# Optimization experiments

Measured on AMD Instinct MI355X. Metric: run time of the kernel, lower is better.

## Reference

```python
import jax, jax.numpy as jnp
import numpy as np

B, H, S, D = 4, 16, 2048, 64


def setup_inputs() -> dict:
    key = jax.random.key(0)
    kq, kk, kv = jax.random.split(key, 3)
    q = jax.random.normal(kq, (B, H, S, D), dtype=jnp.float32)
    k = jax.random.normal(kk, (B, H, S, D), dtype=jnp.float32)
    v = jax.random.normal(kv, (B, H, S, D), dtype=jnp.float32)
    return {"q": q, "k": k, "v": v}


def reference(q, k, v):
    d_k = q.shape[-1]
    scale = 1.0 / jnp.sqrt(jnp.asarray(d_k, dtype=q.dtype))
    # scores: [B, H, S_q, S_k]
    scores = jnp.einsum("bhqd,bhkd->bhqk", q, k) * scale
    attn = jax.nn.softmax(scores, axis=-1)
    out = jnp.einsum("bhqk,bhkd->bhqd", attn, v)
    return out
```

## Files before the change

### kernel.cpp

```cpp
#include <hip/hip_runtime.h>


#define NT 32
#define M0 10.0f

typedef unsigned short u16;
typedef unsigned int   u32;
typedef __bf16 bf16x8 __attribute__((ext_vector_type(8)));
typedef u16    u16x8  __attribute__((ext_vector_type(8)));
typedef u32    u32x4  __attribute__((ext_vector_type(4)));
typedef float  f32x16 __attribute__((ext_vector_type(16)));

__device__ __forceinline__ u16 f2bf(float f) {
    union { float f; u32 u; } x; x.f = f;
    u32 r = x.u + 0x7FFFu + ((x.u >> 16) & 1u);
    return (u16)(r >> 16);
}
__device__ __forceinline__ u32 cvt_pk_bf16(float lo, float hi) {
    u32 r; asm("v_cvt_pk_bf16_f32 %0, %1, %2" : "=v"(r) : "v"(lo), "v"(hi));
    return r;
}
__device__ __forceinline__ float fexp2(float x) {
    float r; asm("v_exp_f32 %0, %1" : "=v"(r) : "v"(x));
    return r;
}
__device__ __forceinline__ void gload16(const void* g, void* l) {
    __builtin_amdgcn_global_load_lds(
        (const __attribute__((address_space(1))) u32*)g,
        (__attribute__((address_space(3))) u32*)l, 16, 0, 0);
}

__global__ __launch_bounds__(256)
void prepass_kernel(const float* __restrict__ K, const float* __restrict__ V,
                    u16* __restrict__ Kb, u16* __restrict__ Vt)
{
    __shared__ u16 T[64 * 66];
    const int t   = threadIdx.x;
    const int bh  = blockIdx.x >> 5;
    const int s0  = (blockIdx.x & 31) * 64;
    const int row = t >> 2;
    const int c0  = (t & 3) * 16;

    {
        const float* kp = K + ((size_t)bh * 2048 + s0 + row) * 64 + c0;
        #pragma unroll
        for (int i = 0; i < 2; ++i) {
            float4 a = ((const float4*)kp)[2 * i];
            float4 b = ((const float4*)kp)[2 * i + 1];
            u16x8 o;
            o[0] = f2bf(a.x); o[1] = f2bf(a.y); o[2] = f2bf(a.z); o[3] = f2bf(a.w);
            o[4] = f2bf(b.x); o[5] = f2bf(b.y); o[6] = f2bf(b.z); o[7] = f2bf(b.w);
            *(u16x8*)(Kb + ((size_t)bh * 2048 + s0 + row) * 64 + c0 + 8 * i) = o;
        }
    }
    {
        const float* vp = V + ((size_t)bh * 2048 + s0 + row) * 64 + c0;
        #pragma unroll
        for (int i = 0; i < 4; ++i) {
            float4 a = ((const float4*)vp)[i];
            T[(c0 + 4 * i + 0) * 66 + row] = f2bf(a.x);
            T[(c0 + 4 * i + 1) * 66 + row] = f2bf(a.y);
            T[(c0 + 4 * i + 2) * 66 + row] = f2bf(a.z);
            T[(c0 + 4 * i + 3) * 66 + row] = f2bf(a.w);
        }
    }
    __syncthreads();
    {
        const int d  = t >> 2;
        const int k0 = (t & 3) * 16;
        #pragma unroll
        for (int i = 0; i < 2; ++i) {
            u16x8 o;
            #pragma unroll
            for (int j = 0; j < 8; ++j) o[j] = T[d * 66 + k0 + 8 * i + j];
            *(u16x8*)(Vt + ((size_t)bh * 64 + d) * 2048 + s0 + k0 + 8 * i) = o;
        }
    }
}

__global__ __launch_bounds__(256)
void attn_fwd_kernel(const float* __restrict__ Qg, const u16* __restrict__ Kb,
                     const u16* __restrict__ Vt, float* __restrict__ Og)
{
    __shared__ u16 Klds[2][4096];
    __shared__ u16 Vlds[2][4096];

    const int tid = threadIdx.x;
    const int w   = tid >> 6;
    const int l31 = tid & 31;
    const int hi  = (tid & 63) >> 5;
    const int sw  = l31 & 7;

    const int id = (blockIdx.x & 7) * 128 + (blockIdx.x >> 3);
    const int bh = id >> 4;
    const int q0 = (id & 15) * 128;
    const int qr = q0 + w * 32 + l31;

    const size_t baseQ = (size_t)bh * 2048 * 64;
    const u16* kg = Kb + (size_t)bh * 2048 * 64;
    const u16* vg = Vt + (size_t)bh * 64 * 2048;

    const float SCL = 0.125f * 1.44269504088896f;
    bf16x8 bq[4];
    #pragma unroll
    for (int dc = 0; dc < 4; ++dc) {
        const float* qp = Qg + baseQ + (size_t)qr * 64 + dc * 16 + hi * 8;
        float4 a = ((const float4*)qp)[0];
        float4 b = ((const float4*)qp)[1];
        u16x8 t;
        t[0] = f2bf(a.x * SCL); t[1] = f2bf(a.y * SCL);
        t[2] = f2bf(a.z * SCL); t[3] = f2bf(a.w * SCL);
        t[4] = f2bf(b.x * SCL); t[5] = f2bf(b.y * SCL);
        t[6] = f2bf(b.z * SCL); t[7] = f2bf(b.w * SCL);
        bq[dc] = __builtin_bit_cast(bf16x8, t);
    }

    int co[4];
    #pragma unroll
    for (int c = 0; c < 4; ++c) co[c] = ((2 * c + hi) ^ sw) * 8;

    u32x4 onev; onev[0] = 0x3F803F80u; onev[1] = 0x3F803F80u;
    onev[2] = 0x3F803F80u; onev[3] = 0x3F803F80u;
    const bf16x8 bones = __builtin_bit_cast(bf16x8, onev);

    f32x16 acc[2], acc2;
    #pragma unroll
    for (int i = 0; i < 16; ++i) { acc[0][i] = 0.f; acc[1][i] = 0.f; acc2[i] = 0.f; }

    const int srow = tid >> 3;
    const int kc   = ((tid & 7) ^ (srow & 7)) * 8;
    const u16* kS0 = kg + (size_t)srow * 64 + kc;
    const u16* kS1 = kg + (size_t)(srow + 32) * 64 + kc;
    const u16* vS0 = vg + (size_t)srow * 2048 + kc;
    const u16* vS1 = vg + (size_t)(srow + 32) * 2048 + kc;

    auto stage = [&](int t) {
        u16* kd = &Klds[t & 1][tid * 8];
        u16* vd = &Vlds[t & 1][tid * 8];
        const size_t ko = (size_t)t * 4096;
        const size_t vo = (size_t)t * 64;
        gload16(kS0 + ko, kd);
        gload16(kS1 + ko, kd + 2048);
        gload16(vS0 + vo, vd);
        gload16(vS1 + vo, vd + 2048);
    };

    auto compute = [&](const u16* Kl, const u16* Vl) {
        f32x16 sA, sB;
        #pragma unroll
        for (int i = 0; i < 16; ++i) { sA[i] = -M0; sB[i] = -M0; }
        __builtin_amdgcn_s_setprio(1);
        #pragma unroll
        for (int dc = 0; dc < 4; ++dc) {
            bf16x8 ak0 = *(const bf16x8*)(Kl + l31 * 64 + co[dc]);
            bf16x8 ak1 = *(const bf16x8*)(Kl + (32 + l31) * 64 + co[dc]);
            sA = __builtin_amdgcn_mfma_f32_32x32x16_bf16(ak0, bq[dc], sA, 0, 0, 0);
            sB = __builtin_amdgcn_mfma_f32_32x32x16_bf16(ak1, bq[dc], sB, 0, 0, 0);
        }
        __builtin_amdgcn_s_setprio(0);

        #pragma unroll
        for (int i = 0; i < 16; ++i) sA[i] = fexp2(sA[i]);
        #pragma unroll
        for (int i = 0; i < 16; ++i) sB[i] = fexp2(sB[i]);

        u32 wpk[2][8];
        #pragma unroll
        for (int a = 0; a < 8; ++a) {
            wpk[0][a] = cvt_pk_bf16(sA[2 * a], sA[2 * a + 1]);
            wpk[1][a] = cvt_pk_bf16(sB[2 * a], sB[2 * a + 1]);
        }

        __builtin_amdgcn_s_setprio(1);
        #pragma unroll
        for (int ks = 0; ks < 4; ++ks) {
            const int kt = ks >> 1, mb = 4 * (ks & 1);
            u32 f0 = wpk[kt][mb + 0], f2 = wpk[kt][mb + 2];
            u32 f1 = wpk[kt][mb + 1], f3 = wpk[kt][mb + 3];
            asm("v_permlane32_swap_b32 %0, %1" : "+v"(f0), "+v"(f2));
            asm("v_permlane32_swap_b32 %0, %1" : "+v"(f1), "+v"(f3));
            u32x4 fwv; fwv[0] = f0; fwv[1] = f1; fwv[2] = f2; fwv[3] = f3;
            bf16x8 pa = __builtin_bit_cast(bf16x8, fwv);
            bf16x8 bv0 = *(const bf16x8*)(Vl + l31 * 64 + co[ks]);
            bf16x8 bv1 = *(const bf16x8*)(Vl + (32 + l31) * 64 + co[ks]);
            acc[0] = __builtin_amdgcn_mfma_f32_32x32x16_bf16(pa, bv0, acc[0], 0, 0, 0);
            acc[1] = __builtin_amdgcn_mfma_f32_32x32x16_bf16(pa, bv1, acc[1], 0, 0, 0);
            acc2   = __builtin_amdgcn_mfma_f32_32x32x16_bf16(pa, bones, acc2, 0, 0, 0);
        }
        __builtin_amdgcn_s_setprio(0);
    };

    stage(0);
    for (int t = 0; t < NT - 1; ++t) {
        stage(t + 1);
        asm volatile("s_waitcnt vmcnt(4)" ::: "memory");
        __builtin_amdgcn_s_barrier();
        compute(Klds[t & 1], Vlds[t & 1]);
        asm volatile("s_waitcnt lgkmcnt(0)" ::: "memory");
        __builtin_amdgcn_s_barrier();
    }
    asm volatile("s_waitcnt vmcnt(0)" ::: "memory");
    __builtin_amdgcn_s_barrier();
    compute(Klds[(NT - 1) & 1], Vlds[(NT - 1) & 1]);

    #pragma unroll
    for (int r = 0; r < 16; ++r) {
        int cr = (r & 3) + 8 * (r >> 2) + 4 * hi;
        float inv = 1.0f / acc2[r];
        size_t o = baseQ + (size_t)(q0 + w * 32 + cr) * 64 + l31;
        Og[o]      = acc[0][r] * inv;
        Og[o + 32] = acc[1][r] * inv;
    }
}

extern "C" void kernel_launch(void* const* d_in, const int* in_sizes, int n_in,
                              void* d_out, int out_size, void* d_ws, size_t ws_size,
                              hipStream_t stream) {
    const float* q = (const float*)d_in[0];
    const float* k = (const float*)d_in[1];
    const float* v = (const float*)d_in[2];
    float* o = (float*)d_out;
    u16* kb = (u16*)d_ws;
    u16* vt = kb + (size_t)64 * 2048 * 64;
    prepass_kernel<<<dim3(2048), dim3(256), 0, stream>>>(k, v, kb, vt);
    attn_fwd_kernel<<<dim3(1024), dim3(256), 0, stream>>>(q, kb, vt, o);
}
```

Baseline: 114.2 us.

## Process 64 query rows per wave and stage K/V through registers

Each wave now handles two 32-row query groups (256 queries per block, 512 blocks), so every K and V fragment read from LDS feeds twice as many MFMAs. The direct global-to-LDS loads are replaced by register prefetch followed by LDS writes and __syncthreads. The goal is to halve K/V LDS and global traffic per query and raise MFMA density. The cost is doubled accumulator registers, lower occupancy, fewer blocks than before on the GPU, and a different load pipeline.

New measurement: 122.9 us. 1.08x slower.

```diff
diff --git a/kernel.cpp b/kernel.cpp
--- a/kernel.cpp
+++ b/kernel.cpp
@@ -23,11 +23,6 @@
 __device__ __forceinline__ float fexp2(float x) {
     float r; asm("v_exp_f32 %0, %1" : "=v"(r) : "v"(x));
     return r;
-}
-__device__ __forceinline__ void gload16(const void* g, void* l) {
-    __builtin_amdgcn_global_load_lds(
-        (const __attribute__((address_space(1))) u32*)g,
-        (__attribute__((address_space(3))) u32*)l, 16, 0, 0);
 }
 
 __global__ __launch_bounds__(256)
@@ -91,20 +86,22 @@
     const int hi  = (tid & 63) >> 5;
     const int sw  = l31 & 7;
 
-    const int id = (blockIdx.x & 7) * 128 + (blockIdx.x >> 3);
-    const int bh = id >> 4;
-    const int q0 = (id & 15) * 128;
-    const int qr = q0 + w * 32 + l31;
+    const int id = (blockIdx.x & 7) * 64 + (blockIdx.x >> 3);
+    const int bh = id >> 3;
+    const int q0 = (id & 7) * 256;
+    const int qw = q0 + w * 64;
 
     const size_t baseQ = (size_t)bh * 2048 * 64;
     const u16* kg = Kb + (size_t)bh * 2048 * 64;
     const u16* vg = Vt + (size_t)bh * 64 * 2048;
 
     const float SCL = 0.125f * 1.44269504088896f;
-    bf16x8 bq[4];
-    #pragma unroll
-    for (int dc = 0; dc < 4; ++dc) {
-        const float* qp = Qg + baseQ + (size_t)qr * 64 + dc * 16 + hi * 8;
+    bf16x8 bq[2][4];
+    #pragma unroll
+    for (int qg = 0; qg < 2; ++qg)
+      #pragma unroll
+      for (int dc = 0; dc < 4; ++dc) {
+        const float* qp = Qg + baseQ + (size_t)(qw + qg * 32 + l31) * 64 + dc * 16 + hi * 8;
         float4 a = ((const float4*)qp)[0];
         float4 b = ((const float4*)qp)[1];
         u16x8 t;
@@ -112,8 +109,8 @@
         t[2] = f2bf(a.z * SCL); t[3] = f2bf(a.w * SCL);
         t[4] = f2bf(b.x * SCL); t[5] = f2bf(b.y * SCL);
         t[6] = f2bf(b.z * SCL); t[7] = f2bf(b.w * SCL);
-        bq[dc] = __builtin_bit_cast(bf16x8, t);
-    }
+        bq[qg][dc] = __builtin_bit_cast(bf16x8, t);
+      }
 
     int co[4];
     #pragma unroll
@@ -123,9 +120,18 @@
     onev[2] = 0x3F803F80u; onev[3] = 0x3F803F80u;
     const bf16x8 bones = __builtin_bit_cast(bf16x8, onev);
 
-    f32x16 acc[2], acc2;
-    #pragma unroll
-    for (int i = 0; i < 16; ++i) { acc[0][i] = 0.f; acc[1][i] = 0.f; acc2[i] = 0.f; }
+    f32x16 acc[2][2];
+    f32x16 acc2[2];
+    #pragma unroll
+    for (int qg = 0; qg < 2; ++qg) {
+      acc2[qg] = (f32x16){0.f};
+      #pragma unroll
+      for (int dt = 0; dt < 2; ++dt)
+        #pragma unroll
+        for (int i = 0; i < 16; ++i) acc[qg][dt][i] = 0.f;
+      #pragma unroll
+      for (int i = 0; i < 16; ++i) acc2[qg][i] = 0.f;
+    }
 
     const int srow = tid >> 3;
     const int kc   = ((tid & 7) ^ (srow & 7)) * 8;
@@ -134,82 +140,103 @@
     const u16* vS0 = vg + (size_t)srow * 2048 + kc;
     const u16* vS1 = vg + (size_t)(srow + 32) * 2048 + kc;
 
-    auto stage = [&](int t) {
+    u16x8 rA, rB, rC, rD;
+    auto load_tile = [&](int t) {
+        rA = *(const u16x8*)(kS0 + (size_t)t * 4096);
+        rB = *(const u16x8*)(kS1 + (size_t)t * 4096);
+        rC = *(const u16x8*)(vS0 + (size_t)t * 64);
+        rD = *(const u16x8*)(vS1 + (size_t)t * 64);
+    };
+    auto write_tile = [&](int t) {
         u16* kd = &Klds[t & 1][tid * 8];
         u16* vd = &Vlds[t & 1][tid * 8];
-        const size_t ko = (size_t)t * 4096;
-        const size_t vo = (size_t)t * 64;
-        gload16(kS0 + ko, kd);
-        gload16(kS1 + ko, kd + 2048);
-        gload16(vS0 + vo, vd);
-        gload16(vS1 + vo, vd + 2048);
+        *(u16x8*)kd = rA;
+        *(u16x8*)(kd + 2048) = rB;
+        *(u16x8*)vd = rC;
+        *(u16x8*)(vd + 2048) = rD;
     };
 
     auto compute = [&](const u16* Kl, const u16* Vl) {
-        f32x16 sA, sB;
-        #pragma unroll
-        for (int i = 0; i < 16; ++i) { sA[i] = -M0; sB[i] = -M0; }
-        __builtin_amdgcn_s_setprio(1);
-        #pragma unroll
-        for (int dc = 0; dc < 4; ++dc) {
-            bf16x8 ak0 = *(const bf16x8*)(Kl + l31 * 64 + co[dc]);
-            bf16x8 ak1 = *(const bf16x8*)(Kl + (32 + l31) * 64 + co[dc]);
-            sA = __builtin_amdgcn_mfma_f32_32x32x16_bf16(ak0, bq[dc], sA, 0, 0, 0);
-            sB = __builtin_amdgcn_mfma_f32_32x32x16_bf16(ak1, bq[dc], sB, 0, 0, 0);
-        }
-        __builtin_amdgcn_s_setprio(0);
-
-        #pragma unroll
-        for (int i = 0; i < 16; ++i) sA[i] = fexp2(sA[i]);
-        #pragma unroll
-        for (int i = 0; i < 16; ++i) sB[i] = fexp2(sB[i]);
-
-        u32 wpk[2][8];
-        #pragma unroll
-        for (int a = 0; a < 8; ++a) {
-            wpk[0][a] = cvt_pk_bf16(sA[2 * a], sA[2 * a + 1]);
-            wpk[1][a] = cvt_pk_bf16(sB[2 * a], sB[2 * a + 1]);
-        }
-
-        __builtin_amdgcn_s_setprio(1);
-        #pragma unroll
-        for (int ks = 0; ks < 4; ++ks) {
-            const int kt = ks >> 1, mb = 4 * (ks & 1);
-            u32 f0 = wpk[kt][mb + 0], f2 = wpk[kt][mb + 2];
-            u32 f1 = wpk[kt][mb + 1], f3 = wpk[kt][mb + 3];
-            asm("v_permlane32_swap_b32 %0, %1" : "+v"(f0), "+v"(f2));
-            asm("v_permlane32_swap_b32 %0, %1" : "+v"(f1), "+v"(f3));
-            u32x4 fwv; fwv[0] = f0; fwv[1] = f1; fwv[2] = f2; fwv[3] = f3;
-            bf16x8 pa = __builtin_bit_cast(bf16x8, fwv);
-            bf16x8 bv0 = *(const bf16x8*)(Vl + l31 * 64 + co[ks]);
-            bf16x8 bv1 = *(const bf16x8*)(Vl + (32 + l31) * 64 + co[ks]);
-            acc[0] = __builtin_amdgcn_mfma_f32_32x32x16_bf16(pa, bv0, acc[0], 0, 0, 0);
-            acc[1] = __builtin_amdgcn_mfma_f32_32x32x16_bf16(pa, bv1, acc[1], 0, 0, 0);
-            acc2   = __builtin_amdgcn_mfma_f32_32x32x16_bf16(pa, bones, acc2, 0, 0, 0);
-        }
-        __builtin_amdgcn_s_setprio(0);
+        #pragma unroll
+        for (int kh = 0; kh < 2; ++kh) {
+            f32x16 s0, s1;
+            #pragma unroll
+            for (int i = 0; i < 16; ++i) { s0[i] = -M0; s1[i] = -M0; }
+            __builtin_amdgcn_s_setprio(1);
+            #pragma unroll
+            for (int dc = 0; dc < 4; ++dc) {
+                bf16x8 ak = *(const bf16x8*)(Kl + (kh * 32 + l31) * 64 + co[dc]);
+                s0 = __builtin_amdgcn_mfma_f32_32x32x16_bf16(ak, bq[0][dc], s0, 0, 0, 0);
+                s1 = __builtin_amdgcn_mfma_f32_32x32x16_bf16(ak, bq[1][dc], s1, 0, 0, 0);
+            }
+            __builtin_amdgcn_s_setprio(0);
+
+            #pragma unroll
+            for (int i = 0; i < 16; ++i) s0[i] = fexp2(s0[i]);
+            #pragma unroll
+            for (int i = 0; i < 16; ++i) s1[i] = fexp2(s1[i]);
+
+            u32 w0[8], w1[8];
+            #pragma unroll
+            for (int a = 0; a < 8; ++a) {
+                w0[a] = cvt_pk_bf16(s0[2 * a], s0[2 * a + 1]);
+                w1[a] = cvt_pk_bf16(s1[2 * a], s1[2 * a + 1]);
+            }
+
+            __builtin_amdgcn_s_setprio(1);
+            #pragma unroll
+            for (int ki = 0; ki < 2; ++ki) {
+                const int ks = kh * 2 + ki, mb = 4 * ki;
+                u32 a0 = w0[mb + 0], a2 = w0[mb + 2];
+                u32 a1 = w0[mb + 1], a3 = w0[mb + 3];
+                asm("v_permlane32_swap_b32 %0, %1" : "+v"(a0), "+v"(a2));
+                asm("v_permlane32_swap_b32 %0, %1" : "+v"(a1), "+v"(a3));
+                u32x4 fw0; fw0[0] = a0; fw0[1] = a1; fw0[2] = a2; fw0[3] = a3;
+                bf16x8 pa0 = __builtin_bit_cast(bf16x8, fw0);
+                u32 b0 = w1[mb + 0], b2 = w1[mb + 2];
+                u32 b1 = w1[mb + 1], b3 = w1[mb + 3];
+                asm("v_permlane32_swap_b32 %0, %1" : "+v"(b0), "+v"(b2));
+                asm("v_permlane32_swap_b32 %0, %1" : "+v"(b1), "+v"(b3));
+                u32x4 fw1; fw1[0] = b0; fw1[1] = b1; fw1[2] = b2; fw1[3] = b3;
+                bf16x8 pa1 = __builtin_bit_cast(bf16x8, fw1);
+
+                bf16x8 bv0 = *(const bf16x8*)(Vl + l31 * 64 + co[ks]);
+                bf16x8 bv1 = *(const bf16x8*)(Vl + (32 + l31) * 64 + co[ks]);
+                acc[0][0] = __builtin_amdgcn_mfma_f32_32x32x16_bf16(pa0, bv0, acc[0][0], 0, 0, 0);
+                acc[0][1] = __builtin_amdgcn_mfma_f32_32x32x16_bf16(pa0, bv1, acc[0][1], 0, 0, 0);
+                acc[1][0] = __builtin_amdgcn_mfma_f32_32x32x16_bf16(pa1, bv0, acc[1][0], 0, 0, 0);
+                acc[1][1] = __builtin_amdgcn_mfma_f32_32x32x16_bf16(pa1, bv1, acc[1][1], 0, 0, 0);
+                acc2[0]   = __builtin_amdgcn_mfma_f32_32x32x16_bf16(pa0, bones, acc2[0], 0, 0, 0);
+                acc2[1]   = __builtin_amdgcn_mfma_f32_32x32x16_bf16(pa1, bones, acc2[1], 0, 0, 0);
+            }
+            __builtin_amdgcn_s_setprio(0);
+            __builtin_amdgcn_sched_barrier(0);
+        }
     };
 
-    stage(0);
-    for (int t = 0; t < NT - 1; ++t) {
-        stage(t + 1);
-        asm volatile("s_waitcnt vmcnt(4)" ::: "memory");
-        __builtin_amdgcn_s_barrier();
+    load_tile(0);
+    write_tile(0);
+    __syncthreads();
+    for (int t = 0; t < NT; ++t) {
+        if (t + 1 < NT) load_tile(t + 1);
         compute(Klds[t & 1], Vlds[t & 1]);
-        asm volatile("s_waitcnt lgkmcnt(0)" ::: "memory");
-        __builtin_amdgcn_s_barrier();
-    }
-    asm volatile("s_waitcnt vmcnt(0)" ::: "memory");
-    __builtin_amdgcn_s_barrier();
-    compute(Klds[(NT - 1) & 1], Vlds[(NT - 1) & 1]);
+        if (t + 1 < NT) {
+            write_tile(t + 1);
+            __syncthreads();
+        }
+    }
 
     #pragma unroll
     for (int r = 0; r < 16; ++r) {
         int cr = (r & 3) + 8 * (r >> 2) + 4 * hi;
-        float inv = 1.0f / acc2[r];
-        size_t o = baseQ + (size_t)(q0 + w * 32 + cr) * 64 + l31;
-        Og[o]      = acc[0][r] * inv;
-        Og[o + 32] = acc[1][r] * inv;
+        float inv0 = 1.0f / acc2[0][r];
+        float inv1 = 1.0f / acc2[1][r];
+        size_t o0 = baseQ + (size_t)(qw + cr) * 64 + l31;
+        size_t o1 = baseQ + (size_t)(qw + 32 + cr) * 64 + l31;
+        Og[o0]      = acc[0][0][r] * inv0;
+        Og[o0 + 32] = acc[0][1][r] * inv0;
+        Og[o1]      = acc[1][0][r] * inv1;
+        Og[o1 + 32] = acc[1][1][r] * inv1;
     }
 }
 
@@ -223,5 +250,5 @@
     u16* kb = (u16*)d_ws;
     u16* vt = kb + (size_t)64 * 2048 * 64;
     prepass_kernel<<<dim3(2048), dim3(256), 0, stream>>>(k, v, kb, vt);
-    attn_fwd_kernel<<<dim3(1024), dim3(256), 0, stream>>>(q, kb, vt, o);
-}
+    attn_fwd_kernel<<<dim3(512), dim3(256), 0, stream>>>(q, kb, vt, o);
+}
```
